# Kernel optimization log

Hardware: AMD Instinct MI355X
Metric: run time of the kernel (lower is better)

Reference implementation:

```python
import jax, jax.numpy as jnp
import numpy as np
from jax import lax

A = -0.75  # torch bicubic cubic-kernel coefficient

def _cubic(t):
    t = jnp.abs(t)
    return jnp.where(t <= 1.0, ((A + 2.0) * t - (A + 3.0)) * t * t + 1.0,
                     jnp.where(t < 2.0, A * (((t - 5.0) * t + 8.0) * t - 4.0), 0.0))

def _up2_1d(x, axis):
    # torch F.interpolate(scale_factor=2, mode='bicubic', align_corners=False) along one axis
    n = x.shape[axis]
    src = (jnp.arange(2 * n, dtype=jnp.float32) + 0.5) / 2.0 - 0.5
    i0 = jnp.floor(src).astype(jnp.int32)
    taps = i0[:, None] + jnp.arange(-1, 3)          # [2n,4]
    w = _cubic(src[:, None] - taps.astype(jnp.float32))
    g = jnp.take(x, jnp.clip(taps, 0, n - 1), axis=axis)  # clamp = border replicate
    wshape = [1] * g.ndim
    wshape[axis] = 2 * n
    wshape[axis + 1] = 4
    return jnp.sum(g * w.reshape(wshape), axis=axis + 1)

def bicubic_x2(x):
    return _up2_1d(_up2_1d(x, 2), 3)

def conv2d(x, w, b, stride=1, pad=0):
    y = lax.conv_general_dilated(x, w, (stride, stride), [(pad, pad), (pad, pad)],
                                 dimension_numbers=('NCHW', 'OIHW', 'NCHW'))
    return y + b[None, :, None, None]

def lrelu(x):
    return jax.nn.leaky_relu(x, 0.2)

def resblock(x, w1, b1, w2, b2):
    return x + conv2d(jax.nn.relu(conv2d(x, w1, b1, pad=1)), w2, b2, pad=1)

def feat_head(x, cw, cb, rw1, rb1, rw2, rb2):
    # Conv2d(3,32,5,p=2) -> LReLU -> ResBlock(32) -> LReLU
    return lrelu(resblock(lrelu(conv2d(x, cw, cb, pad=2)), rw1, rb1, rw2, rb2))

def setup_inputs() -> dict:
    key = jax.random.key(0)
    ks = jax.random.split(key, 16)
    def w(k, shape):
        fan = shape[1] * shape[2] * shape[3]
        return jax.random.normal(k, shape, jnp.float32) / np.sqrt(fan)
    def bvec(k, n):
        return jax.random.normal(k, (n,), jnp.float32) * 0.01
    return {
        'x':     jax.random.normal(ks[0], (1, 64, 320, 320), jnp.float32),
        'query': jax.random.normal(ks[1], (1, 3, 160, 160), jnp.float32),
        'ref':   jax.random.normal(ks[2], (1, 3, 320, 320), jnp.float32),
        'conv1_w': w(ks[3], (32, 3, 5, 5)),   'conv1_b': bvec(ks[4], 32),
        'r1_w1':   w(ks[5], (32, 32, 3, 3)),  'r1_b1':   bvec(ks[6], 32),
        'r1_w2':   w(ks[7], (32, 32, 3, 3)),  'r1_b2':   bvec(ks[8], 32),
        'p1_w':    w(ks[9], (32, 64, 5, 5)),  'p1_b':    bvec(ks[10], 32),
        'pr_w1':   w(ks[11], (32, 32, 3, 3)), 'pr_b1':   bvec(ks[12], 32),
        'pr_w2':   w(ks[13], (32, 32, 3, 3)), 'pr_b2':   bvec(ks[14], 32),
        'p2_w':    w(ks[15], (3, 32, 1, 1)),  'p2_b':    jnp.zeros((3,), jnp.float32),
    }

def reference(x, query, ref, conv1_w, conv1_b, r1_w1, r1_b1, r1_w2, r1_b2,
              p1_w, p1_b, pr_w1, pr_b1, pr_w2, pr_b2, p2_w, p2_b):
    ks = 2
    qf = feat_head(bicubic_x2(query), conv1_w, conv1_b, r1_w1, r1_b1, r1_w2, r1_b2)
    rf = feat_head(ref, conv1_w, conv1_b, r1_w1, r1_b1, r1_w2, r1_b2)
    feat = jnp.concatenate([rf, qf], axis=1)  # [b,64,h,w]
    hid = lrelu(resblock(lrelu(conv2d(feat, p1_w, p1_b, pad=2)), pr_w1, pr_b1, pr_w2, pr_b2))
    affine = conv2d(hid, p2_w, p2_b, pad=0) + 1.0   # [b,3,h,w]
    affine = jnp.clip(affine, -3.0, 3.0)
    xp = jnp.pad(x, ((0, 0), (0, 0), (1, 1), (1, 1)), mode='reflect')
    b, c, hp, wp = xp.shape
    h, w = affine.shape[2], affine.shape[3]
    aff = jnp.transpose(affine, (0, 2, 3, 1))       # [b,h,w,3]
    s_x, s_y = aff[..., 0:1], aff[..., 1:2]
    theta = (aff[..., 2:3] - 1.0) * 1.0472          # +/- 60 degrees
    # kernel grid (ks=2): meshgrid('ij') of [-0.5, 0.5], flattened
    pn_x = jnp.array([-0.5, -0.5, 0.5, 0.5], dtype=xp.dtype)
    pn_y = jnp.array([-0.5, 0.5, -0.5, 0.5], dtype=xp.dtype)
    px = pn_x * s_x                                  # [b,h,w,4]
    py = pn_y * s_y
    ct, st = jnp.cos(theta), jnp.sin(theta)
    # [px,py] @ [[c, s],[-s, c]]
    rx = px * ct - py * st
    ry = px * st + py * ct
    off = (ks - 1) // 2 + 0.5                        # 0.5
    p0x = jnp.arange(1, h + 1, dtype=xp.dtype)[None, :, None, None]
    p0y = jnp.arange(1, w + 1, dtype=xp.dtype)[None, None, :, None]
    p_x = rx + off + p0x
    p_y = ry + off + p0y
    lt_x = jnp.floor(lax.stop_gradient(p_x))
    lt_y = jnp.floor(lax.stop_gradient(p_y))
    rb_x, rb_y = lt_x + 1.0, lt_y + 1.0
    lt_xc = jnp.clip(lt_x, 0, hp - 1); lt_yc = jnp.clip(lt_y, 0, wp - 1)
    rb_xc = jnp.clip(rb_x, 0, hp - 1); rb_yc = jnp.clip(rb_y, 0, wp - 1)
    p_x = jnp.clip(p_x, 0, hp - 1); p_y = jnp.clip(p_y, 0, wp - 1)
    g_lt = (1.0 + lt_xc - p_x) * (1.0 + lt_yc - p_y)
    g_rb = (1.0 - (rb_xc - p_x)) * (1.0 - (rb_yc - p_y))
    g_lb = (1.0 + lt_xc - p_x) * (1.0 - (rb_yc - p_y))
    g_rt = (1.0 - (rb_xc - p_x)) * (1.0 + lt_yc - p_y)
    x_flat = xp.reshape(b, c, hp * wp)
    def gather(qx, qy):
        idx = qx.astype(jnp.int32) * wp + qy.astype(jnp.int32)  # [b,h,w,4]
        return jax.vmap(lambda xf, ix: xf[:, ix])(x_flat, idx)   # [b,c,h,w,4]
    align = (g_lt[:, None] * gather(lt_xc, lt_yc)
             + g_rb[:, None] * gather(rb_xc, rb_yc)
             + g_lb[:, None] * gather(lt_xc, rb_yc)
             + g_rt[:, None] * gather(rb_xc, lt_yc))
    # pixel-shuffle style reshape: N index = ix*ks + iy (from 'ij' meshgrid)
    out = align.reshape(b, c, h, w, ks, ks).transpose(0, 1, 2, 4, 3, 5).reshape(b, c, h * ks, w * ks)
    return out
```

## Files before the change

kernel.cpp:

```cpp
#include <hip/hip_runtime.h>

#define H 320
#define W 320
#define HW (H * W)
#define CH 64

typedef _Float16 f16;
typedef _Float16 f16x8 __attribute__((ext_vector_type(8)));
typedef float f32x16 __attribute__((ext_vector_type(16)));

__device__ __forceinline__ float cubw(float t) {
    t = fabsf(t);
    if (t <= 1.f) return (1.25f * t - 2.25f) * t * t + 1.f;
    if (t < 2.f)  return -0.75f * (((t - 5.f) * t + 8.f) * t - 4.f);
    return 0.f;
}

__device__ __forceinline__ float bicub(const float* __restrict__ qc, int gy, int gx) {
    float sy = gy * 0.5f - 0.25f;
    float sx = gx * 0.5f - 0.25f;
    int iy0 = (int)floorf(sy), ix0 = (int)floorf(sx);
    float o = 0.f;
#pragma unroll
    for (int b = 0; b < 4; b++) {
        int tx = ix0 - 1 + b;
        float wxv = cubw(sx - (float)tx);
        int txc = min(max(tx, 0), 159);
        float s = 0.f;
#pragma unroll
        for (int a = 0; a < 4; a++) {
            int ty = iy0 - 1 + a;
            float wyv = cubw(sy - (float)ty);
            int tyc = min(max(ty, 0), 159);
            s += wyv * qc[tyc * 160 + txc];
        }
        o += wxv * s;
    }
    return o;
}

__global__ __launch_bounds__(256) void repack_k(const float* __restrict__ w0,
                                                const float* __restrict__ w1,
                                                const float* __restrict__ w2,
                                                const float* __restrict__ w3,
                                                const float* __restrict__ w4,
                                                const float* __restrict__ w5,
                                                f16* __restrict__ dst) {
    int li = blockIdx.x * 256 + threadIdx.x;
    if (li >= 11328) return;
    if (li >= 11008) {
        int rel = li - 11008;
        int kc = rel >> 6, l = rel & 63;
        int oc = l & 31, kh = l >> 5;
#pragma unroll
        for (int i = 0; i < 8; ++i) {
            int k = kc * 16 + kh * 8 + i;
            f16 v = (f16)0.f;
            if (k < 75) {
                int tap = k / 3, ic = k - 3 * tap;
                v = (f16)w5[(oc * 3 + ic) * 25 + tap];
            }
            dst[88064 + rel * 8 + i] = v;
        }
        return;
    }
    const float* src;
    int CIN, KS2, base, rel;
    if (li < 1152)       { src = w0; CIN = 32; KS2 = 9;  base = 0;     rel = li; }
    else if (li < 2304)  { src = w1; CIN = 32; KS2 = 9;  base = 9216;  rel = li - 1152; }
    else if (li < 3456)  { src = w2; CIN = 32; KS2 = 9;  base = 18432; rel = li - 2304; }
    else if (li < 4608)  { src = w3; CIN = 32; KS2 = 9;  base = 27648; rel = li - 3456; }
    else                 { src = w4; CIN = 64; KS2 = 25; base = 36864; rel = li - 4608; }
    int fi = rel >> 6, l = rel & 63;
    int kc = fi / KS2, t = fi - kc * KS2;
    int oc = l & 31, kh = l >> 5;
#pragma unroll
    for (int i = 0; i < 8; ++i) {
        int ic = kc * 16 + kh * 8 + i;
        dst[base + rel * 8 + i] = (f16)src[(oc * CIN + ic) * KS2 + t];
    }
}

__global__ __launch_bounds__(256) void hconv_m(const float* __restrict__ query,
                                               const float* __restrict__ ref,
                                               const f16* __restrict__ wr5,
                                               const float* __restrict__ bias,
                                               f16* __restrict__ out) {
    __shared__ float tile[3][12][40];
    const int b = blockIdx.x >= 400 ? 1 : 0;
    const int tb = blockIdx.x - b * 400;
    f16* o = out + (size_t)b * (32 * HW);
    const int x0 = (tb % 10) * 32, y0 = (tb / 10) * 8;
    const int tid = threadIdx.x;

    for (int idx = tid; idx < 1440; idx += 256) {
        int ic = idx / 480;
        int rem = idx - ic * 480;
        int r = rem / 40, c = rem - r * 40;
        int gy = y0 - 2 + r, gx = x0 - 2 + c;
        float v = 0.f;
        if (gy >= 0 && gy < H && gx >= 0 && gx < W)
            v = b ? ref[ic * HW + gy * W + gx]
                  : bicub(query + ic * 25600, gy, gx);
        tile[ic][r][c] = v;
    }
    __syncthreads();

    const int lane = tid & 63, wv = tid >> 6;
    const int R = lane & 31, hh = lane >> 5;

    f32x16 acc0, acc1;
#pragma unroll
    for (int j = 0; j < 16; ++j) { acc0[j] = 0.f; acc1[j] = 0.f; }

#pragma unroll
    for (int kc = 0; kc < 5; ++kc) {
        f16x8 B = *reinterpret_cast<const f16x8*>(wr5 + (kc * 64 + lane) * 8);
#pragma unroll
        for (int m = 0; m < 2; ++m) {
            f16x8 A;
#pragma unroll
            for (int i = 0; i < 8; ++i) {
                int k = kc * 16 + hh * 8 + i;
                float v = 0.f;
                if (k < 75) {
                    int tap = k / 3, ic = k - 3 * tap;
                    int dy = tap / 5, dx = tap - 5 * dy;
                    v = tile[ic][2 * wv + m + dy][R + dx];
                }
                A[i] = (f16)v;
            }
            if (m == 0) acc0 = __builtin_amdgcn_mfma_f32_32x32x16_f16(A, B, acc0, 0, 0, 0);
            else        acc1 = __builtin_amdgcn_mfma_f32_32x32x16_f16(A, B, acc1, 0, 0, 0);
        }
    }

    const float bv = bias[R];
#pragma unroll
    for (int m = 0; m < 2; ++m) {
        const int gy = y0 + 2 * wv + m;
        f32x16 a = m ? acc1 : acc0;
#pragma unroll
        for (int r = 0; r < 16; ++r) {
            int X = x0 + (r & 3) + 8 * (r >> 2) + 4 * hh;
            float v = a[r] + bv;
            v = (v > 0.f) ? v : 0.2f * v;
            o[(gy * W + X) * 32 + R] = (f16)v;
        }
    }
}

template <int KS, int CIN, int ACT, bool RES, int R2W>
__global__ __launch_bounds__(256) void mconv_k(const f16* __restrict__ in,
                                               const f16* __restrict__ wrep,
                                               const float* __restrict__ bias,
                                               const f16* __restrict__ res,
                                               f16* __restrict__ out,
                                               int OUTC, int inStr, int resStr,
                                               int outStr, int oc0Base, int oc0Step) {
    constexpr int PAD = KS / 2;
    constexpr int TROWS = 4 * R2W;
    constexpr int TY = TROWS + 2 * PAD;
    constexpr int TX = 32 + 2 * PAD;
    constexpr int NPX = TY * TX;
    constexpr int NU = CIN / 4;
    constexpr int UM = NU - 1;
    constexpr int KC = CIN / 16;
    constexpr int KS2 = KS * KS;
    constexpr int BPB = 800 / R2W;

    __shared__ uint2 lds2[NPX * NU];

    const int b = blockIdx.x >= BPB ? 1 : 0;
    const int tb = blockIdx.x - b * BPB;
    in  += (size_t)b * inStr;
    res += (size_t)b * resStr;
    out += (size_t)b * outStr;
    const int oc0 = oc0Base + b * oc0Step;

    const int tid = threadIdx.x;
    const int bx = tb % 10;
    const int by = tb / 10;
    const int x0 = bx * 32, y0 = by * TROWS;

    {
        const int cu = tid & UM;
        constexpr int STEP = 256 / NU;
        for (int p = tid / NU; p < NPX; p += STEP) {
            int ly = p / TX, lx = p - ly * TX;
            int gy = y0 - PAD + ly, gx = x0 - PAD + lx;
            uint2 v; v.x = 0u; v.y = 0u;
            if (gy >= 0 && gy < H && gx >= 0 && gx < W)
                v = *reinterpret_cast<const uint2*>(in + (gy * W + gx) * CIN + cu * 4);
            lds2[p * NU + (cu ^ (p & UM))] = v;
        }
    }
    __syncthreads();

    const int lane = tid & 63;
    const int wv = tid >> 6;
    const int R = lane & 31;
    const int hh = lane >> 5;

    f32x16 acc0, acc1;
#pragma unroll
    for (int j = 0; j < 16; ++j) { acc0[j] = 0.f; acc1[j] = 0.f; }

#pragma unroll
    for (int kc = 0; kc < KC; ++kc) {
#pragma unroll
        for (int t = 0; t < KS2; ++t) {
            const int dy = t / KS, dx = t - dy * KS;
            f16x8 B = *reinterpret_cast<const f16x8*>(
                wrep + ((kc * KS2 + t) * 64 + lane) * 8);
            const int u0 = (kc * 2 + hh) * 2;
            {
                int p = (R2W * wv + 0 + dy) * TX + R + dx;
                union { uint2 u[2]; f16x8 v; } A;
                A.u[0] = lds2[p * NU + ((u0)     ^ (p & UM))];
                A.u[1] = lds2[p * NU + ((u0 + 1) ^ (p & UM))];
                acc0 = __builtin_amdgcn_mfma_f32_32x32x16_f16(A.v, B, acc0, 0, 0, 0);
            }
            if constexpr (R2W == 2) {
                int p = (R2W * wv + 1 + dy) * TX + R + dx;
                union { uint2 u[2]; f16x8 v; } A;
                A.u[0] = lds2[p * NU + ((u0)     ^ (p & UM))];
                A.u[1] = lds2[p * NU + ((u0 + 1) ^ (p & UM))];
                acc1 = __builtin_amdgcn_mfma_f32_32x32x16_f16(A.v, B, acc1, 0, 0, 0);
            }
        }
    }

    const float bv = bias[R];
#pragma unroll
    for (int m = 0; m < R2W; ++m) {
        const int gy = y0 + R2W * wv + m;
        f32x16 a = m ? acc1 : acc0;
#pragma unroll
        for (int r = 0; r < 16; ++r) {
            int X = x0 + (r & 3) + 8 * (r >> 2) + 4 * hh;
            int pix = gy * W + X;
            float v = a[r] + bv;
            if constexpr (RES) v += (float)res[pix * 32 + R];
            if constexpr (ACT == 0) v = fmaxf(v, 0.f);
            else                    v = (v > 0.f) ? v : 0.2f * v;
            out[pix * OUTC + oc0 + R] = (f16)v;
        }
    }
}

__global__ __launch_bounds__(256) void affine_k(const f16* __restrict__ hid,
                                                const float* __restrict__ w,
                                                const float* __restrict__ b,
                                                float* __restrict__ outp) {
    int p = blockIdx.x * 256 + threadIdx.x;
    if (p >= HW) return;
    const f16x8* hv = reinterpret_cast<const f16x8*>(hid + p * 32);
    float a0 = 0.f, a1 = 0.f, a2 = 0.f;
#pragma unroll
    for (int cc = 0; cc < 4; ++cc) {
        f16x8 hb = hv[cc];
#pragma unroll
        for (int j = 0; j < 8; ++j) {
            float hval = (float)hb[j];
            int c = cc * 8 + j;
            a0 += hval * w[c];
            a1 += hval * w[32 + c];
            a2 += hval * w[64 + c];
        }
    }
    a0 = fminf(fmaxf(a0 + b[0] + 1.f, -3.f), 3.f);
    a1 = fminf(fmaxf(a1 + b[1] + 1.f, -3.f), 3.f);
    a2 = fminf(fmaxf(a2 + b[2] + 1.f, -3.f), 3.f);
    outp[p] = a0;
    outp[HW + p] = a1;
    outp[2 * HW + p] = a2;
}

__device__ __forceinline__ int reflmap(int q) {
    int s = q - 1;
    if (s < 0) s = -s;
    else if (s > 319) s = 638 - s;
    return s;
}

__global__ __launch_bounds__(256) void sample_k(const float* __restrict__ x,
                                                const float* __restrict__ aff,
                                                float* __restrict__ outp) {
    __shared__ float tile[8 * 6 * 80];
    int bid = blockIdx.x;
    bid = (bid & 7) * 1600 + (bid >> 3);
    const int cg = bid / 1600;
    const int tb = bid - cg * 1600;
    const int h = tb / 5;
    const int q = tb - 5 * h;
    const int tid = threadIdx.x;
    const int ow = q * 128 + (tid & 127);
    const int oh = 2 * h + (tid >> 7);

    const int w = ow >> 1;
    const int ky = ow & 1, kx = oh & 1;
    const int p = h * W + w;
    float s_x = aff[p];
    float s_y = aff[HW + p];
    float th = (aff[2 * HW + p] - 1.f) * 1.0472f;
    float pnx = kx ? 0.5f : -0.5f;
    float pny = ky ? 0.5f : -0.5f;
    float px = pnx * s_x, py = pny * s_y;
    float st, ct;
    __sincosf(th, &st, &ct);
    float rx = px * ct - py * st;
    float ry = px * st + py * ct;
    float p_x = rx + 0.5f + (float)(h + 1);
    float p_y = ry + 0.5f + (float)(w + 1);
    float ltx = floorf(p_x), lty = floorf(p_y);
    float rbx = ltx + 1.f, rby = lty + 1.f;
    float ltxc = fminf(fmaxf(ltx, 0.f), 321.f);
    float ltyc = fminf(fmaxf(lty, 0.f), 321.f);
    float rbxc = fminf(fmaxf(rbx, 0.f), 321.f);
    float rbyc = fminf(fmaxf(rby, 0.f), 321.f);
    p_x = fminf(fmaxf(p_x, 0.f), 321.f);
    p_y = fminf(fmaxf(p_y, 0.f), 321.f);
    float gx0 = 1.f + ltxc - p_x;
    float gx1 = 1.f - (rbxc - p_x);
    float gy0 = 1.f + ltyc - p_y;
    float gy1 = 1.f - (rbyc - p_y);
    float g_lt = gx0 * gy0, g_rb = gx1 * gy1, g_lb = gx0 * gy1, g_rt = gx1 * gy0;
    int ix0 = reflmap((int)ltxc), ix1 = reflmap((int)rbxc);
    int iy0 = reflmap((int)ltyc), iy1 = reflmap((int)rbyc);

    const int rowbase = h - 2;
    const int colbase = q * 64 - 4;
    const int o00 = (ix0 - rowbase) * 80 + (iy0 - colbase);
    const int o01 = (ix0 - rowbase) * 80 + (iy1 - colbase);
    const int o10 = (ix1 - rowbase) * 80 + (iy0 - colbase);
    const int o11 = (ix1 - rowbase) * 80 + (iy1 - colbase);
    const int obase = oh * 640 + ow;
    const int ch0 = cg * 8;

    for (int idx = tid; idx < 864; idx += 256) {
        int ch = idx / 108;
        int rem = idx - ch * 108;
        int row = rem / 18;
        int g = rem - row * 18;
        int rv = rowbase + row;
        int cv = colbase + 4 * g;
        float4 v = make_float4(0.f, 0.f, 0.f, 0.f);
        if (rv >= 0 && rv < H && cv >= 0 && cv < W)
            v = *reinterpret_cast<const float4*>(x + (size_t)(ch0 + ch) * HW + rv * W + cv);
        *reinterpret_cast<float4*>(&tile[ch * 480 + row * 80 + 4 * g]) = v;
    }
    __syncthreads();

#pragma unroll
    for (int c = 0; c < 8; ++c) {
        const float* t = tile + c * 480;
        float v = g_lt * t[o00] + g_rb * t[o11] + g_lb * t[o01] + g_rt * t[o10];
        __builtin_nontemporal_store(v, outp + (size_t)(ch0 + c) * (640 * 640) + obase);
    }
}

extern "C" void kernel_launch(void* const* d_in, const int* in_sizes, int n_in,
                              void* d_out, int out_size, void* d_ws, size_t ws_size,
                              hipStream_t stream) {
    const float* x       = (const float*)d_in[0];
    const float* query   = (const float*)d_in[1];
    const float* ref     = (const float*)d_in[2];
    const float* conv1_w = (const float*)d_in[3];
    const float* conv1_b = (const float*)d_in[4];
    const float* r1_w1   = (const float*)d_in[5];
    const float* r1_b1   = (const float*)d_in[6];
    const float* r1_w2   = (const float*)d_in[7];
    const float* r1_b2   = (const float*)d_in[8];
    const float* p1_w    = (const float*)d_in[9];
    const float* p1_b    = (const float*)d_in[10];
    const float* pr_w1   = (const float*)d_in[11];
    const float* pr_b1   = (const float*)d_in[12];
    const float* pr_w2   = (const float*)d_in[13];
    const float* pr_b2   = (const float*)d_in[14];
    const float* p2_w    = (const float*)d_in[15];
    const float* p2_b    = (const float*)d_in[16];

    float* outp = (float*)d_out;
    float* ws = (float*)d_ws;

    float* affine = ws;
    f16* feat = (f16*)outp;
    f16* Bt   = (f16*)(outp + 32 * HW);
    f16* Ct   = (f16*)(outp + 64 * HW);
    f16* Dt   = (f16*)(outp + 96 * HW);
    f16* wrep = (f16*)(outp + 112 * HW);

    repack_k<<<45, 256, 0, stream>>>(r1_w1, r1_w2, pr_w1, pr_w2, p1_w, conv1_w, wrep);

    hconv_m<<<800, 256, 0, stream>>>(query, ref, wrep + 88064, conv1_b, Bt);
    mconv_k<3, 32, 0, false, 1><<<1600, 256, 0, stream>>>(Bt, wrep,        r1_b1, nullptr, Ct,
                                                          32, 32 * HW, 0, 32 * HW, 0, 0);
    mconv_k<3, 32, 1, true , 1><<<1600, 256, 0, stream>>>(Ct, wrep + 9216, r1_b2, Bt, feat,
                                                          64, 32 * HW, 32 * HW, 0, 32, -32);

    mconv_k<5, 64, 1, false, 2><<<400, 256, 0, stream>>>(feat, wrep + 36864, p1_b, nullptr, Bt,
                                                         32, 0, 0, 0, 0, 0);
    mconv_k<3, 32, 0, false, 1><<<800, 256, 0, stream>>>(Bt, wrep + 18432, pr_b1, nullptr, Ct,
                                                         32, 0, 0, 0, 0, 0);
    mconv_k<3, 32, 1, true , 1><<<800, 256, 0, stream>>>(Ct, wrep + 27648, pr_b2, Bt, Dt,
                                                         32, 0, 0, 0, 0, 0);

    affine_k<<<400, 256, 0, stream>>>(Dt, p2_w, p2_b, affine);

    sample_k<<<12800, 256, 0, stream>>>(x, affine, outp);
}
```

Measured before the change: 267.4 us.

## Fold weight repack into first conv and fuse affine head into last conv

Removes the separate repack launch: the first conv kernel gets extra blocks that repack the later conv weights, and each thread builds its own conv1 B fragments directly from the fp32 weights. The 1x1 affine head is fused into the epilogue of the last residual conv using cross-lane shuffle reductions, which removes a kernel launch and a re-read of the hidden tensor. The 5x5 conv also moves from two rows per wave to one row per wave with twice the blocks. The costs are redundant per-block weight conversion, extra shuffles in the epilogue, and more halo reloads for the 5x5 conv.

```diff
diff --git a/kernel.cpp b/kernel.cpp
--- a/kernel.cpp
+++ b/kernel.cpp
@@ -39,59 +39,62 @@
     return o;
 }
 
-__global__ __launch_bounds__(256) void repack_k(const float* __restrict__ w0,
-                                                const float* __restrict__ w1,
-                                                const float* __restrict__ w2,
-                                                const float* __restrict__ w3,
-                                                const float* __restrict__ w4,
-                                                const float* __restrict__ w5,
-                                                f16* __restrict__ dst) {
-    int li = blockIdx.x * 256 + threadIdx.x;
-    if (li >= 11328) return;
-    if (li >= 11008) {
-        int rel = li - 11008;
-        int kc = rel >> 6, l = rel & 63;
-        int oc = l & 31, kh = l >> 5;
-#pragma unroll
-        for (int i = 0; i < 8; ++i) {
-            int k = kc * 16 + kh * 8 + i;
-            f16 v = (f16)0.f;
-            if (k < 75) {
-                int tap = k / 3, ic = k - 3 * tap;
-                v = (f16)w5[(oc * 3 + ic) * 25 + tap];
-            }
-            dst[88064 + rel * 8 + i] = v;
-        }
-        return;
-    }
-    const float* src;
-    int CIN, KS2, base, rel;
-    if (li < 1152)       { src = w0; CIN = 32; KS2 = 9;  base = 0;     rel = li; }
-    else if (li < 2304)  { src = w1; CIN = 32; KS2 = 9;  base = 9216;  rel = li - 1152; }
-    else if (li < 3456)  { src = w2; CIN = 32; KS2 = 9;  base = 18432; rel = li - 2304; }
-    else if (li < 4608)  { src = w3; CIN = 32; KS2 = 9;  base = 27648; rel = li - 3456; }
-    else                 { src = w4; CIN = 64; KS2 = 25; base = 36864; rel = li - 4608; }
-    int fi = rel >> 6, l = rel & 63;
-    int kc = fi / KS2, t = fi - kc * KS2;
-    int oc = l & 31, kh = l >> 5;
-#pragma unroll
-    for (int i = 0; i < 8; ++i) {
-        int ic = kc * 16 + kh * 8 + i;
-        dst[base + rel * 8 + i] = (f16)src[(oc * CIN + ic) * KS2 + t];
-    }
-}
-
 __global__ __launch_bounds__(256) void hconv_m(const float* __restrict__ query,
                                                const float* __restrict__ ref,
-                                               const f16* __restrict__ wr5,
+                                               const float* __restrict__ conv1_w,
                                                const float* __restrict__ bias,
+                                               const float* __restrict__ w0,
+                                               const float* __restrict__ w1,
+                                               const float* __restrict__ w2,
+                                               const float* __restrict__ w3,
+                                               const float* __restrict__ w4,
+                                               f16* __restrict__ wrep,
                                                f16* __restrict__ out) {
     __shared__ float tile[3][12][40];
+    const int tid = threadIdx.x;
+
+    if (blockIdx.x >= 800) {
+        int li = (blockIdx.x - 800) * 256 + tid;
+        if (li >= 11008) return;
+        const float* src;
+        int CIN, KS2, base, rel;
+        if (li < 1152)       { src = w0; CIN = 32; KS2 = 9;  base = 0;     rel = li; }
+        else if (li < 2304)  { src = w1; CIN = 32; KS2 = 9;  base = 9216;  rel = li - 1152; }
+        else if (li < 3456)  { src = w2; CIN = 32; KS2 = 9;  base = 18432; rel = li - 2304; }
+        else if (li < 4608)  { src = w3; CIN = 32; KS2 = 9;  base = 27648; rel = li - 3456; }
+        else                 { src = w4; CIN = 64; KS2 = 25; base = 36864; rel = li - 4608; }
+        int fi = rel >> 6, l = rel & 63;
+        int kc = fi / KS2, t = fi - kc * KS2;
+        int oc = l & 31, kh = l >> 5;
+#pragma unroll
+        for (int i = 0; i < 8; ++i) {
+            int ic = kc * 16 + kh * 8 + i;
+            wrep[base + rel * 8 + i] = (f16)src[(oc * CIN + ic) * KS2 + t];
+        }
+        return;
+    }
+
     const int b = blockIdx.x >= 400 ? 1 : 0;
     const int tb = blockIdx.x - b * 400;
     f16* o = out + (size_t)b * (32 * HW);
     const int x0 = (tb % 10) * 32, y0 = (tb / 10) * 8;
-    const int tid = threadIdx.x;
+
+    const int lane = tid & 63, wv = tid >> 6;
+    const int R = lane & 31, hh = lane >> 5;
+
+    f16x8 bw[5];
+#pragma unroll
+    for (int kc = 0; kc < 5; ++kc)
+#pragma unroll
+        for (int i = 0; i < 8; ++i) {
+            int k = kc * 16 + hh * 8 + i;
+            f16 v = (f16)0.f;
+            if (k < 75) {
+                int tap = k / 3, ic = k - 3 * tap;
+                v = (f16)conv1_w[(R * 3 + ic) * 25 + tap];
+            }
+            bw[kc][i] = v;
+        }
 
     for (int idx = tid; idx < 1440; idx += 256) {
         int ic = idx / 480;
@@ -106,16 +109,12 @@
     }
     __syncthreads();
 
-    const int lane = tid & 63, wv = tid >> 6;
-    const int R = lane & 31, hh = lane >> 5;
-
     f32x16 acc0, acc1;
 #pragma unroll
     for (int j = 0; j < 16; ++j) { acc0[j] = 0.f; acc1[j] = 0.f; }
 
 #pragma unroll
     for (int kc = 0; kc < 5; ++kc) {
-        f16x8 B = *reinterpret_cast<const f16x8*>(wr5 + (kc * 64 + lane) * 8);
 #pragma unroll
         for (int m = 0; m < 2; ++m) {
             f16x8 A;
@@ -130,8 +129,8 @@
                 }
                 A[i] = (f16)v;
             }
-            if (m == 0) acc0 = __builtin_amdgcn_mfma_f32_32x32x16_f16(A, B, acc0, 0, 0, 0);
-            else        acc1 = __builtin_amdgcn_mfma_f32_32x32x16_f16(A, B, acc1, 0, 0, 0);
+            if (m == 0) acc0 = __builtin_amdgcn_mfma_f32_32x32x16_f16(A, bw[kc], acc0, 0, 0, 0);
+            else        acc1 = __builtin_amdgcn_mfma_f32_32x32x16_f16(A, bw[kc], acc1, 0, 0, 0);
         }
     }
 
@@ -150,14 +149,17 @@
     }
 }
 
-template <int KS, int CIN, int ACT, bool RES, int R2W>
+template <int KS, int CIN, int ACT, bool RES, int R2W, bool AFF>
 __global__ __launch_bounds__(256) void mconv_k(const f16* __restrict__ in,
                                                const f16* __restrict__ wrep,
                                                const float* __restrict__ bias,
                                                const f16* __restrict__ res,
                                                f16* __restrict__ out,
                                                int OUTC, int inStr, int resStr,
-                                               int outStr, int oc0Base, int oc0Step) {
+                                               int outStr, int oc0Base, int oc0Step,
+                                               const float* __restrict__ aw,
+                                               const float* __restrict__ ab,
+                                               float* __restrict__ affout) {
     constexpr int PAD = KS / 2;
     constexpr int TROWS = 4 * R2W;
     constexpr int TY = TROWS + 2 * PAD;
@@ -244,37 +246,27 @@
             if constexpr (RES) v += (float)res[pix * 32 + R];
             if constexpr (ACT == 0) v = fmaxf(v, 0.f);
             else                    v = (v > 0.f) ? v : 0.2f * v;
-            out[pix * OUTC + oc0 + R] = (f16)v;
-        }
-    }
-}
-
-__global__ __launch_bounds__(256) void affine_k(const f16* __restrict__ hid,
-                                                const float* __restrict__ w,
-                                                const float* __restrict__ b,
-                                                float* __restrict__ outp) {
-    int p = blockIdx.x * 256 + threadIdx.x;
-    if (p >= HW) return;
-    const f16x8* hv = reinterpret_cast<const f16x8*>(hid + p * 32);
-    float a0 = 0.f, a1 = 0.f, a2 = 0.f;
-#pragma unroll
-    for (int cc = 0; cc < 4; ++cc) {
-        f16x8 hb = hv[cc];
-#pragma unroll
-        for (int j = 0; j < 8; ++j) {
-            float hval = (float)hb[j];
-            int c = cc * 8 + j;
-            a0 += hval * w[c];
-            a1 += hval * w[32 + c];
-            a2 += hval * w[64 + c];
-        }
-    }
-    a0 = fminf(fmaxf(a0 + b[0] + 1.f, -3.f), 3.f);
-    a1 = fminf(fmaxf(a1 + b[1] + 1.f, -3.f), 3.f);
-    a2 = fminf(fmaxf(a2 + b[2] + 1.f, -3.f), 3.f);
-    outp[p] = a0;
-    outp[HW + p] = a1;
-    outp[2 * HW + p] = a2;
+            f16 vq = (f16)v;
+            out[pix * OUTC + oc0 + R] = vq;
+            if constexpr (AFF) {
+                float vh = (float)vq;
+                float s0 = vh * aw[R];
+                float s1 = vh * aw[32 + R];
+                float s2 = vh * aw[64 + R];
+#pragma unroll
+                for (int msk = 16; msk >= 1; msk >>= 1) {
+                    s0 += __shfl_xor(s0, msk);
+                    s1 += __shfl_xor(s1, msk);
+                    s2 += __shfl_xor(s2, msk);
+                }
+                if (R == 0) {
+                    affout[pix]          = fminf(fmaxf(s0 + ab[0] + 1.f, -3.f), 3.f);
+                    affout[HW + pix]     = fminf(fmaxf(s1 + ab[1] + 1.f, -3.f), 3.f);
+                    affout[2 * HW + pix] = fminf(fmaxf(s2 + ab[2] + 1.f, -3.f), 3.f);
+                }
+            }
+        }
+    }
 }
 
 __device__ __forceinline__ int reflmap(int q) {
@@ -391,22 +383,25 @@
     f16* Dt   = (f16*)(outp + 96 * HW);
     f16* wrep = (f16*)(outp + 112 * HW);
 
-    repack_k<<<45, 256, 0, stream>>>(r1_w1, r1_w2, pr_w1, pr_w2, p1_w, conv1_w, wrep);
-
-    hconv_m<<<800, 256, 0, stream>>>(query, ref, wrep + 88064, conv1_b, Bt);
-    mconv_k<3, 32, 0, false, 1><<<1600, 256, 0, stream>>>(Bt, wrep,        r1_b1, nullptr, Ct,
-                                                          32, 32 * HW, 0, 32 * HW, 0, 0);
-    mconv_k<3, 32, 1, true , 1><<<1600, 256, 0, stream>>>(Ct, wrep + 9216, r1_b2, Bt, feat,
-                                                          64, 32 * HW, 32 * HW, 0, 32, -32);
-
-    mconv_k<5, 64, 1, false, 2><<<400, 256, 0, stream>>>(feat, wrep + 36864, p1_b, nullptr, Bt,
-                                                         32, 0, 0, 0, 0, 0);
-    mconv_k<3, 32, 0, false, 1><<<800, 256, 0, stream>>>(Bt, wrep + 18432, pr_b1, nullptr, Ct,
-                                                         32, 0, 0, 0, 0, 0);
-    mconv_k<3, 32, 1, true , 1><<<800, 256, 0, stream>>>(Ct, wrep + 27648, pr_b2, Bt, Dt,
-                                                         32, 0, 0, 0, 0, 0);
-
-    affine_k<<<400, 256, 0, stream>>>(Dt, p2_w, p2_b, affine);
+    hconv_m<<<843, 256, 0, stream>>>(query, ref, conv1_w, conv1_b,
+                                     r1_w1, r1_w2, pr_w1, pr_w2, p1_w, wrep, Bt);
+
+    mconv_k<3, 32, 0, false, 1, false><<<1600, 256, 0, stream>>>(
+        Bt, wrep,        r1_b1, nullptr, Ct, 32, 32 * HW, 0, 32 * HW, 0, 0,
+        nullptr, nullptr, nullptr);
+    mconv_k<3, 32, 1, true , 1, false><<<1600, 256, 0, stream>>>(
+        Ct, wrep + 9216, r1_b2, Bt, feat, 64, 32 * HW, 32 * HW, 0, 32, -32,
+        nullptr, nullptr, nullptr);
+
+    mconv_k<5, 64, 1, false, 1, false><<<800, 256, 0, stream>>>(
+        feat, wrep + 36864, p1_b, nullptr, Bt, 32, 0, 0, 0, 0, 0,
+        nullptr, nullptr, nullptr);
+    mconv_k<3, 32, 0, false, 1, false><<<800, 256, 0, stream>>>(
+        Bt, wrep + 18432, pr_b1, nullptr, Ct, 32, 0, 0, 0, 0, 0,
+        nullptr, nullptr, nullptr);
+    mconv_k<3, 32, 1, true , 1, true ><<<800, 256, 0, stream>>>(
+        Ct, wrep + 27648, pr_b2, Bt, Dt, 32, 0, 0, 0, 0, 0,
+        p2_w, p2_b, affine);
 
     sample_k<<<12800, 256, 0, stream>>>(x, affine, outp);
 }
```

Result: slower. 281.0 us (+5.1%).

## Fuse weight repack into first conv and make bicubic upsample separable

Applied to the files above, without the earlier changes.

Removes the standalone repack kernel launch. Extra blocks of the first conv kernel now do the weight repacking, and each block builds its own conv1 weights straight into registers from the fp32 tensor. The bicubic upsampling of the query is split into two passes through shared memory: a horizontal pass with precomputed tap weights and indices, then a vertical pass. This replaces 16 gathered taps per pixel. The changes save a launch and redundant arithmetic and loads, at the cost of extra shared memory and barriers.

```diff
diff --git a/kernel.cpp b/kernel.cpp
--- a/kernel.cpp
+++ b/kernel.cpp
@@ -16,106 +16,139 @@
     return 0.f;
 }
 
-__device__ __forceinline__ float bicub(const float* __restrict__ qc, int gy, int gx) {
-    float sy = gy * 0.5f - 0.25f;
-    float sx = gx * 0.5f - 0.25f;
-    int iy0 = (int)floorf(sy), ix0 = (int)floorf(sx);
-    float o = 0.f;
-#pragma unroll
-    for (int b = 0; b < 4; b++) {
-        int tx = ix0 - 1 + b;
-        float wxv = cubw(sx - (float)tx);
-        int txc = min(max(tx, 0), 159);
-        float s = 0.f;
-#pragma unroll
-        for (int a = 0; a < 4; a++) {
-            int ty = iy0 - 1 + a;
-            float wyv = cubw(sy - (float)ty);
-            int tyc = min(max(ty, 0), 159);
-            s += wyv * qc[tyc * 160 + txc];
-        }
-        o += wxv * s;
-    }
-    return o;
-}
-
-__global__ __launch_bounds__(256) void repack_k(const float* __restrict__ w0,
-                                                const float* __restrict__ w1,
-                                                const float* __restrict__ w2,
-                                                const float* __restrict__ w3,
-                                                const float* __restrict__ w4,
-                                                const float* __restrict__ w5,
-                                                f16* __restrict__ dst) {
-    int li = blockIdx.x * 256 + threadIdx.x;
-    if (li >= 11328) return;
-    if (li >= 11008) {
-        int rel = li - 11008;
-        int kc = rel >> 6, l = rel & 63;
-        int oc = l & 31, kh = l >> 5;
-#pragma unroll
-        for (int i = 0; i < 8; ++i) {
-            int k = kc * 16 + kh * 8 + i;
-            f16 v = (f16)0.f;
-            if (k < 75) {
-                int tap = k / 3, ic = k - 3 * tap;
-                v = (f16)w5[(oc * 3 + ic) * 25 + tap];
-            }
-            dst[88064 + rel * 8 + i] = v;
-        }
-        return;
-    }
-    const float* src;
-    int CIN, KS2, base, rel;
-    if (li < 1152)       { src = w0; CIN = 32; KS2 = 9;  base = 0;     rel = li; }
-    else if (li < 2304)  { src = w1; CIN = 32; KS2 = 9;  base = 9216;  rel = li - 1152; }
-    else if (li < 3456)  { src = w2; CIN = 32; KS2 = 9;  base = 18432; rel = li - 2304; }
-    else if (li < 4608)  { src = w3; CIN = 32; KS2 = 9;  base = 27648; rel = li - 3456; }
-    else                 { src = w4; CIN = 64; KS2 = 25; base = 36864; rel = li - 4608; }
-    int fi = rel >> 6, l = rel & 63;
-    int kc = fi / KS2, t = fi - kc * KS2;
-    int oc = l & 31, kh = l >> 5;
-#pragma unroll
-    for (int i = 0; i < 8; ++i) {
-        int ic = kc * 16 + kh * 8 + i;
-        dst[base + rel * 8 + i] = (f16)src[(oc * CIN + ic) * KS2 + t];
-    }
-}
-
 __global__ __launch_bounds__(256) void hconv_m(const float* __restrict__ query,
                                                const float* __restrict__ ref,
-                                               const f16* __restrict__ wr5,
+                                               const float* __restrict__ conv1_w,
                                                const float* __restrict__ bias,
+                                               const float* __restrict__ w0,
+                                               const float* __restrict__ w1,
+                                               const float* __restrict__ w2,
+                                               const float* __restrict__ w3,
+                                               const float* __restrict__ w4,
+                                               f16* __restrict__ wrep,
                                                f16* __restrict__ out) {
     __shared__ float tile[3][12][40];
+    __shared__ float hbuf[3][10][40];
+    __shared__ float wxt[40][4];
+    __shared__ int   txt[40][4];
+    __shared__ float wyt[12][4];
+    __shared__ int   tyb[12];
+    const int tid = threadIdx.x;
+
+    if (blockIdx.x >= 800) {
+        int li = (blockIdx.x - 800) * 256 + tid;
+        if (li >= 11008) return;
+        const float* src;
+        int CIN, KS2, base, rel;
+        if (li < 1152)       { src = w0; CIN = 32; KS2 = 9;  base = 0;     rel = li; }
+        else if (li < 2304)  { src = w1; CIN = 32; KS2 = 9;  base = 9216;  rel = li - 1152; }
+        else if (li < 3456)  { src = w2; CIN = 32; KS2 = 9;  base = 18432; rel = li - 2304; }
+        else if (li < 4608)  { src = w3; CIN = 32; KS2 = 9;  base = 27648; rel = li - 3456; }
+        else                 { src = w4; CIN = 64; KS2 = 25; base = 36864; rel = li - 4608; }
+        int fi = rel >> 6, l = rel & 63;
+        int kc = fi / KS2, t = fi - kc * KS2;
+        int oc = l & 31, kh = l >> 5;
+#pragma unroll
+        for (int i = 0; i < 8; ++i) {
+            int ic = kc * 16 + kh * 8 + i;
+            wrep[base + rel * 8 + i] = (f16)src[(oc * CIN + ic) * KS2 + t];
+        }
+        return;
+    }
+
     const int b = blockIdx.x >= 400 ? 1 : 0;
     const int tb = blockIdx.x - b * 400;
     f16* o = out + (size_t)b * (32 * HW);
     const int x0 = (tb % 10) * 32, y0 = (tb / 10) * 8;
-    const int tid = threadIdx.x;
-
-    for (int idx = tid; idx < 1440; idx += 256) {
-        int ic = idx / 480;
-        int rem = idx - ic * 480;
-        int r = rem / 40, c = rem - r * 40;
-        int gy = y0 - 2 + r, gx = x0 - 2 + c;
-        float v = 0.f;
-        if (gy >= 0 && gy < H && gx >= 0 && gx < W)
-            v = b ? ref[ic * HW + gy * W + gx]
-                  : bicub(query + ic * 25600, gy, gx);
-        tile[ic][r][c] = v;
-    }
-    __syncthreads();
 
     const int lane = tid & 63, wv = tid >> 6;
     const int R = lane & 31, hh = lane >> 5;
 
+    f16x8 bw[5];
+#pragma unroll
+    for (int kc = 0; kc < 5; ++kc)
+#pragma unroll
+        for (int i = 0; i < 8; ++i) {
+            int k = kc * 16 + hh * 8 + i;
+            f16 v = (f16)0.f;
+            if (k < 75) {
+                int tap = k / 3, ic = k - 3 * tap;
+                v = (f16)conv1_w[(R * 3 + ic) * 25 + tap];
+            }
+            bw[kc][i] = v;
+        }
+
+    if (b) {
+        for (int idx = tid; idx < 1440; idx += 256) {
+            int ic = idx / 480;
+            int rem = idx - ic * 480;
+            int r = rem / 40, c = rem - r * 40;
+            int gy = y0 - 2 + r, gx = x0 - 2 + c;
+            float v = 0.f;
+            if (gy >= 0 && gy < H && gx >= 0 && gx < W)
+                v = ref[ic * HW + gy * W + gx];
+            tile[ic][r][c] = v;
+        }
+        __syncthreads();
+    } else {
+        const int rbase = y0 / 2 - 3;
+        if (tid < 40) {
+            int gx = x0 - 2 + tid;
+            float sx = gx * 0.5f - 0.25f;
+            int ix0 = (int)floorf(sx);
+#pragma unroll
+            for (int a = 0; a < 4; ++a) {
+                int tx = ix0 - 1 + a;
+                wxt[tid][a] = cubw(sx - (float)tx);
+                txt[tid][a] = min(max(tx, 0), 159);
+            }
+        } else if (tid < 52) {
+            int r = tid - 40;
+            int gy = y0 - 2 + r;
+            float sy = gy * 0.5f - 0.25f;
+            int iy0 = (int)floorf(sy);
+            tyb[r] = iy0 - 1 - rbase;
+#pragma unroll
+            for (int a = 0; a < 4; ++a)
+                wyt[r][a] = cubw(sy - (float)(iy0 - 1 + a));
+        }
+        __syncthreads();
+        for (int idx = tid; idx < 1200; idx += 256) {
+            int ic = idx / 400;
+            int rem = idx - ic * 400;
+            int r = rem / 40, c = rem - r * 40;
+            int qr = min(max(rbase + r, 0), 159);
+            const float* qrow = query + ic * 25600 + qr * 160;
+            hbuf[ic][r][c] = wxt[c][0] * qrow[txt[c][0]]
+                           + wxt[c][1] * qrow[txt[c][1]]
+                           + wxt[c][2] * qrow[txt[c][2]]
+                           + wxt[c][3] * qrow[txt[c][3]];
+        }
+        __syncthreads();
+        for (int idx = tid; idx < 1440; idx += 256) {
+            int ic = idx / 480;
+            int rem = idx - ic * 480;
+            int r = rem / 40, c = rem - r * 40;
+            int gy = y0 - 2 + r, gx = x0 - 2 + c;
+            float v = 0.f;
+            if (gy >= 0 && gy < H && gx >= 0 && gx < W) {
+                int tb0 = tyb[r];
+                v = wyt[r][0] * hbuf[ic][tb0][c]
+                  + wyt[r][1] * hbuf[ic][tb0 + 1][c]
+                  + wyt[r][2] * hbuf[ic][tb0 + 2][c]
+                  + wyt[r][3] * hbuf[ic][tb0 + 3][c];
+            }
+            tile[ic][r][c] = v;
+        }
+        __syncthreads();
+    }
+
     f32x16 acc0, acc1;
 #pragma unroll
     for (int j = 0; j < 16; ++j) { acc0[j] = 0.f; acc1[j] = 0.f; }
 
 #pragma unroll
     for (int kc = 0; kc < 5; ++kc) {
-        f16x8 B = *reinterpret_cast<const f16x8*>(wr5 + (kc * 64 + lane) * 8);
 #pragma unroll
         for (int m = 0; m < 2; ++m) {
             f16x8 A;
@@ -130,8 +163,8 @@
                 }
                 A[i] = (f16)v;
             }
-            if (m == 0) acc0 = __builtin_amdgcn_mfma_f32_32x32x16_f16(A, B, acc0, 0, 0, 0);
-            else        acc1 = __builtin_amdgcn_mfma_f32_32x32x16_f16(A, B, acc1, 0, 0, 0);
+            if (m == 0) acc0 = __builtin_amdgcn_mfma_f32_32x32x16_f16(A, bw[kc], acc0, 0, 0, 0);
+            else        acc1 = __builtin_amdgcn_mfma_f32_32x32x16_f16(A, bw[kc], acc1, 0, 0, 0);
         }
     }
 
@@ -391,20 +424,20 @@
     f16* Dt   = (f16*)(outp + 96 * HW);
     f16* wrep = (f16*)(outp + 112 * HW);
 
-    repack_k<<<45, 256, 0, stream>>>(r1_w1, r1_w2, pr_w1, pr_w2, p1_w, conv1_w, wrep);
-
-    hconv_m<<<800, 256, 0, stream>>>(query, ref, wrep + 88064, conv1_b, Bt);
-    mconv_k<3, 32, 0, false, 1><<<1600, 256, 0, stream>>>(Bt, wrep,        r1_b1, nullptr, Ct,
-                                                          32, 32 * HW, 0, 32 * HW, 0, 0);
-    mconv_k<3, 32, 1, true , 1><<<1600, 256, 0, stream>>>(Ct, wrep + 9216, r1_b2, Bt, feat,
-                                                          64, 32 * HW, 32 * HW, 0, 32, -32);
-
-    mconv_k<5, 64, 1, false, 2><<<400, 256, 0, stream>>>(feat, wrep + 36864, p1_b, nullptr, Bt,
-                                                         32, 0, 0, 0, 0, 0);
-    mconv_k<3, 32, 0, false, 1><<<800, 256, 0, stream>>>(Bt, wrep + 18432, pr_b1, nullptr, Ct,
-                                                         32, 0, 0, 0, 0, 0);
-    mconv_k<3, 32, 1, true , 1><<<800, 256, 0, stream>>>(Ct, wrep + 27648, pr_b2, Bt, Dt,
-                                                         32, 0, 0, 0, 0, 0);
+    hconv_m<<<843, 256, 0, stream>>>(query, ref, conv1_w, conv1_b,
+                                     r1_w1, r1_w2, pr_w1, pr_w2, p1_w, wrep, Bt);
+
+    mconv_k<3, 32, 0, false, 1><<<1600, 256, 0, stream>>>(
+        Bt, wrep,        r1_b1, nullptr, Ct, 32, 32 * HW, 0, 32 * HW, 0, 0);
+    mconv_k<3, 32, 1, true , 1><<<1600, 256, 0, stream>>>(
+        Ct, wrep + 9216, r1_b2, Bt, feat, 64, 32 * HW, 32 * HW, 0, 32, -32);
+
+    mconv_k<5, 64, 1, false, 2><<<400, 256, 0, stream>>>(
+        feat, wrep + 36864, p1_b, nullptr, Bt, 32, 0, 0, 0, 0, 0);
+    mconv_k<3, 32, 0, false, 1><<<800, 256, 0, stream>>>(
+        Bt, wrep + 18432, pr_b1, nullptr, Ct, 32, 0, 0, 0, 0, 0);
+    mconv_k<3, 32, 1, true , 1><<<800, 256, 0, stream>>>(
+        Ct, wrep + 27648, pr_b2, Bt, Dt, 32, 0, 0, 0, 0, 0);
 
     affine_k<<<400, 256, 0, stream>>>(Dt, p2_w, p2_b, affine);
 
```

Result: slower. 275.7 us (+3.1%).
